# Optimization experiments

Hardware: AMD Instinct MI355X
Metric: run time of the kernel (lower is better)

Reference implementation:

```python
import jax, jax.numpy as jnp
import numpy as np

G, N, E, F, D = 4096, 64, 256, 64, 128
H1, H2 = 16, 2
EP = 32768
EPS = 1e-15
MAX_LOGSTD = 10.0


def setup_inputs() -> dict:
    key = jax.random.key(0)
    ks = jax.random.split(key, 16)
    def lin(k, i, o):
        return (jax.random.normal(k, (i, o), jnp.float32) / np.sqrt(i)).astype(jnp.float32)
    inp = {}
    inp["x"] = jax.random.normal(ks[0], (G, N, F), jnp.float32)
    inp["edge_index"] = jax.random.randint(ks[1], (G, 2, E), 0, N, dtype=jnp.int32)
    inp["edge_weight"] = jax.random.uniform(ks[2], (G, E), jnp.float32)
    inp["pos_edges"] = jax.random.randint(ks[3], (2, EP), 0, G, dtype=jnp.int32)
    inp["neg_edges"] = jax.random.randint(ks[4], (2, EP), 0, G, dtype=jnp.int32)
    inp["eps"] = jax.random.normal(ks[5], (G, D), jnp.float32)
    inp["W_gcn1"] = lin(ks[6], F, D); inp["b_gcn1"] = jnp.zeros((D,), jnp.float32)
    inp["W_fc1"] = lin(ks[7], D, H1); inp["b_fc1"] = jnp.zeros((H1,), jnp.float32)
    inp["W_fc2"] = lin(ks[8], H1, H2); inp["b_fc2"] = jnp.zeros((H2,), jnp.float32)
    inp["W_c1"] = lin(ks[9], D, 2 * D); inp["b_c1"] = jnp.zeros((2 * D,), jnp.float32)
    inp["W_mu"] = lin(ks[10], 2 * D, D); inp["b_mu"] = jnp.zeros((D,), jnp.float32)
    inp["W_ls"] = lin(ks[11], 2 * D, D); inp["b_ls"] = jnp.zeros((D,), jnp.float32)
    inp["emb"] = jax.random.normal(ks[12], (G, D), jnp.float32)
    inp["W_lin1"] = lin(ks[13], 2 * D, 2 * D); inp["b_lin1"] = jnp.zeros((2 * D,), jnp.float32)
    inp["W_lin2"] = lin(ks[14], 2 * D, 2 * D); inp["b_lin2"] = jnp.zeros((2 * D,), jnp.float32)
    return inp


def gcn_conv(x, src, dst, w, W, b, n):
    # PyG GCNConv: add self-loops (weight 1), sym-normalize, aggregate at target (col).
    xw = x @ W                                      # [n, out]
    deg = jnp.zeros((n,), xw.dtype).at[dst].add(w) + 1.0
    dinv = jax.lax.rsqrt(deg)
    norm = dinv[src] * w * dinv[dst]
    agg = jnp.zeros_like(xw).at[dst].add(xw[src] * norm[:, None])
    agg = agg + xw * (dinv * dinv)[:, None]         # self-loop term
    return agg + b


def sage_graph(x, ei, w, W_gcn1, b_gcn1, W_fc1, b_fc1, W_fc2, b_fc2):
    src, dst = ei[0], ei[1]
    h = gcn_conv(x, src, dst, w, W_gcn1, b_gcn1, N)          # [N, D]
    a1 = jnp.tanh(h @ W_fc1 + b_fc1)                         # [N, H1]
    S = jax.nn.softmax(a1 @ W_fc2 + b_fc2, axis=1)           # [N, 2]
    # get_laplacian(normalization='sym'): L = I - D^{-1/2} A D^{-1/2}, deg from row
    deg = jnp.zeros((N,), x.dtype).at[src].add(w)
    dinv = jnp.where(deg > 0, jax.lax.rsqrt(jnp.maximum(deg, 1e-30)), 0.0)
    lw = -dinv[src] * w * dinv[dst]
    L = jnp.zeros((N, N), x.dtype).at[src, dst].add(lw) + jnp.eye(N, dtype=x.dtype)
    new_adj = S.T @ (L @ S)                                  # [2, 2]
    norm_adj = new_adj / jnp.maximum(jnp.sum(jnp.abs(new_adj), axis=1, keepdims=True), 1e-12)
    diag = jnp.diagonal(norm_adj)
    pos_penalty = jnp.mean((diag - 1.0) ** 2)                # MSE vs ones(2)
    g_emb = jnp.mean(S.T @ h, axis=0)                        # [D]
    return g_emb, pos_penalty


def gcn_conv_unw(x, src, dst, W, b, n):
    return gcn_conv(x, src, dst, jnp.ones(src.shape, x.dtype), W, b, n)


def reference(x, edge_index, edge_weight, pos_edges, neg_edges, eps,
              W_gcn1, b_gcn1, W_fc1, b_fc1, W_fc2, b_fc2,
              W_c1, b_c1, W_mu, b_mu, W_ls, b_ls, emb,
              W_lin1, b_lin1, W_lin2, b_lin2):
    g_embs, pens = jax.vmap(sage_graph,
                            in_axes=(0, 0, 0, None, None, None, None, None, None))(
        x, edge_index, edge_weight, W_gcn1, b_gcn1, W_fc1, b_fc1, W_fc2, b_fc2)
    positive_penalty = jnp.mean(pens)
    # VGAE encode over graph-level graph (dropout in eval mode = identity)
    ps, pd = pos_edges[0], pos_edges[1]
    h = jax.nn.relu(gcn_conv_unw(g_embs, ps, pd, W_c1, b_c1, G))
    mu = gcn_conv_unw(h, ps, pd, W_mu, b_mu, G)
    logstd = jnp.minimum(gcn_conv_unw(h, ps, pd, W_ls, b_ls, G), MAX_LOGSTD)
    z = mu + eps * jnp.exp(logstd)                            # reparametrize
    zc = jnp.concatenate([emb, z], axis=-1)                   # [G, 2D]
    def pred(ei):
        fx = zc[ei[0]] @ W_lin1 + b_lin1
        fy = zc[ei[1]] @ W_lin2 + b_lin2
        return jax.nn.sigmoid(jnp.sum(fx * fy, axis=1))
    pos_pred = pred(pos_edges)
    neg_pred = pred(neg_edges)
    rec_loss = -jnp.mean(jnp.log(pos_pred + EPS)) - jnp.mean(jnp.log(1.0 - neg_pred + EPS))
    kl = -0.5 * jnp.mean(jnp.sum(1.0 + 2.0 * logstd - mu ** 2 - jnp.exp(2.0 * logstd), axis=1))
    pre_loss = rec_loss + kl / G
    return pre_loss, positive_penalty, pos_pred, neg_pred
```

## Files before the change

### kernel.cpp

```cpp
#include <hip/hip_runtime.h>
#include <hip/hip_bf16.h>
#include <math.h>

#define GG   4096
#define NNODE 64
#define EEDGE 256
#define FFEAT 64
#define DDIM 128
#define EP   32768

__global__ void k_prep(const float* __restrict__ Wg, const float* __restrict__ Wf1,
                       const float* __restrict__ bf1, const float* __restrict__ bg,
                       float* __restrict__ Wgf1, float* __restrict__ bcomb,
                       float* __restrict__ bg32) {
    int t = threadIdx.x;
    for (int o = t; o < 1024; o += 256) {
        int f = o >> 4, j = o & 15;
        float s = 0.f;
        for (int d = 0; d < 128; ++d) s += Wg[f * 128 + d] * Wf1[d * 16 + j];
        Wgf1[o] = s;
    }
    if (t < 16) {
        float s = bf1[t];
        for (int d = 0; d < 128; ++d) s += bg[d] * Wf1[d * 16 + t];
        bcomb[t] = s;
    }
    if (t >= 128) bg32[t - 128] = 32.0f * bg[t - 128];
}

__global__ __launch_bounds__(256) void k_xw(
    const float* __restrict__ x, const float* __restrict__ Wgf1,
    float* __restrict__ xwg)
{
    __shared__ __align__(16) float Ws[1024];
    const int t = threadIdx.x;
    for (int i = t; i < 1024; i += 256) Ws[i] = Wgf1[i];
    __syncthreads();
    const size_t r0 = (size_t)blockIdx.x * 512 + t;
    const float* x0 = x + r0 * 64;
    const float* x1 = x + (r0 + 256) * 64;
    float4 z = {0, 0, 0, 0};
    float4 c00 = z, c01 = z, c02 = z, c03 = z;
    float4 c10 = z, c11 = z, c12 = z, c13 = z;
#pragma unroll
    for (int k4 = 0; k4 < 16; ++k4) {
        float4 a0 = *(const float4*)&x0[k4 * 4];
        float4 a1 = *(const float4*)&x1[k4 * 4];
#define STEP(KK, E) { \
        const float* wr = &Ws[(k4 * 4 + (KK)) * 16]; \
        float4 w0 = *(const float4*)wr,       w1 = *(const float4*)(wr + 4); \
        float4 w2 = *(const float4*)(wr + 8), w3 = *(const float4*)(wr + 12); \
        c00.x += a0.E * w0.x; c00.y += a0.E * w0.y; c00.z += a0.E * w0.z; c00.w += a0.E * w0.w; \
        c01.x += a0.E * w1.x; c01.y += a0.E * w1.y; c01.z += a0.E * w1.z; c01.w += a0.E * w1.w; \
        c02.x += a0.E * w2.x; c02.y += a0.E * w2.y; c02.z += a0.E * w2.z; c02.w += a0.E * w2.w; \
        c03.x += a0.E * w3.x; c03.y += a0.E * w3.y; c03.z += a0.E * w3.z; c03.w += a0.E * w3.w; \
        c10.x += a1.E * w0.x; c10.y += a1.E * w0.y; c10.z += a1.E * w0.z; c10.w += a1.E * w0.w; \
        c11.x += a1.E * w1.x; c11.y += a1.E * w1.y; c11.z += a1.E * w1.z; c11.w += a1.E * w1.w; \
        c12.x += a1.E * w2.x; c12.y += a1.E * w2.y; c12.z += a1.E * w2.z; c12.w += a1.E * w2.w; \
        c13.x += a1.E * w3.x; c13.y += a1.E * w3.y; c13.z += a1.E * w3.z; c13.w += a1.E * w3.w; }
        STEP(0, x) STEP(1, y) STEP(2, z) STEP(3, w)
#undef STEP
    }
    float* o0 = &xwg[r0 * 16];
    *(float4*)&o0[0] = c00; *(float4*)&o0[4] = c01;
    *(float4*)&o0[8] = c02; *(float4*)&o0[12] = c03;
    float* o1 = &xwg[(r0 + 256) * 16];
    *(float4*)&o1[0] = c10; *(float4*)&o1[4] = c11;
    *(float4*)&o1[8] = c12; *(float4*)&o1[12] = c13;
}

__global__ __launch_bounds__(256) void k_pg(
    const float* __restrict__ x, const float* __restrict__ xwg,
    const int* __restrict__ ei, const float* __restrict__ ew,
    const float* __restrict__ bcomb,
    const float* __restrict__ Wf2, const float* __restrict__ bf2,
    float* __restrict__ Qh, float* __restrict__ pens)
{
    __shared__ __align__(16) float sm[4688];
    float* xws   = sm;
    float* a1s   = sm + 1280;
    int*   srcs  = (int*)(sm + 2304);
    int*   dsts  = (int*)(sm + 2560);
    float* lwx   = sm + 2816;
    int*   lsrc  = (int*)(sm + 3072);
    float* lnrm  = sm + 3328;
    float* enrm  = sm + 3584;
    int*   icnt  = (int*)(sm + 3840);
    int*   offs  = (int*)(sm + 3904);
    int*   curs  = (int*)(sm + 3968);
    float* degw  = sm + 4032;
    float* dinvs = sm + 4096;
    float* deg2s = sm + 4160;
    float* dinv2s= sm + 4224;
    float* wv    = sm + 4288;
    float* Ss    = sm + 4352;
    float* Ssum  = sm + 4480;
    float* LSs   = sm + 4544;
    float* bcs   = sm + 4672;

    const int g = blockIdx.x;
    const int t = threadIdx.x;

    const int* eg = ei + (size_t)g * 512;
    const int sR = eg[t];
    const int dR = eg[256 + t];
    const float wR = ew[(size_t)g * 256 + t];
    {
        int n = t >> 2, j4 = (t & 3) * 4;
        float4 v = *(const float4*)&xwg[(size_t)g * 1024 + n * 16 + j4];
        *(float4*)&xws[n * 20 + j4] = v;
    }
    srcs[t] = sR; dsts[t] = dR;
    if (t < 16) bcs[t] = bcomb[t];
    if (t < 64) { icnt[t] = 0; degw[t] = 1.0f; deg2s[t] = 0.0f; }
    if (t < 128) LSs[t] = 0.0f;
    __syncthreads();

    atomicAdd(&icnt[dR], 1);
    atomicAdd(&degw[dR], wR);
    atomicAdd(&deg2s[sR], wR);
    __syncthreads();

    if (t < 64) {
        int v = icnt[t], own = v;
        for (int o = 1; o < 64; o <<= 1) { int u = __shfl_up(v, o); if (t >= o) v += u; }
        int excl = v - own;
        offs[t] = excl; curs[t] = excl;
        dinvs[t] = rsqrtf(degw[t]);
        float dg = deg2s[t];
        dinv2s[t] = dg > 0.0f ? rsqrtf(fmaxf(dg, 1e-30f)) : 0.0f;
    }
    __syncthreads();

    {
        int pos = atomicAdd(&curs[dR], 1);
        float nm = dinvs[sR] * wR * dinvs[dR];
        lsrc[pos] = sR;
        lnrm[pos] = nm;
        enrm[t] = nm;
        lwx[t] = -dinv2s[sR] * wR * dinv2s[dR];
    }
    __syncthreads();

    {
        int n = t >> 2, j4 = (t & 3) * 4;
        float dv = dinvs[n], sc = dv * dv;
        float4 A = *(const float4*)&xws[n * 20 + j4];
        A.x *= sc; A.y *= sc; A.z *= sc; A.w *= sc;
        int o = offs[n], c = icnt[n];
        for (int j = 0; j < c; ++j) {
            int s = lsrc[o + j];
            float nm = lnrm[o + j];
            float4 X = *(const float4*)&xws[s * 20 + j4];
            A.x += X.x * nm; A.y += X.y * nm; A.z += X.z * nm; A.w += X.w * nm;
        }
        float4 bb = *(const float4*)&bcs[j4];
        a1s[n * 16 + j4 + 0] = tanhf(A.x + bb.x);
        a1s[n * 16 + j4 + 1] = tanhf(A.y + bb.y);
        a1s[n * 16 + j4 + 2] = tanhf(A.z + bb.z);
        a1s[n * 16 + j4 + 3] = tanhf(A.w + bb.w);
    }
    __syncthreads();

    if (t < 128) {
        int n = t >> 1, kk = t & 1;
        float z = bf2[kk];
#pragma unroll
        for (int j = 0; j < 16; ++j) z += a1s[n * 16 + j] * Wf2[j * 2 + kk];
        Ss[n * 2 + kk] = z;
    }
    __syncthreads();

    if (t < 64) {
        float z0 = Ss[t * 2], z1 = Ss[t * 2 + 1];
        float m = fmaxf(z0, z1);
        float e0 = expf(z0 - m), e1 = expf(z1 - m);
        float inv = 1.0f / (e0 + e1);
        e0 *= inv; e1 *= inv;
        Ss[t * 2] = e0; Ss[t * 2 + 1] = e1;
        float su = e0 + e1;
        Ssum[t] = su;
        wv[t] = dinvs[t] * dinvs[t] * su;
    }
    __syncthreads();

    for (int i = t; i < 512; i += 256) {
        int e = i >> 1, kk = i & 1;
        atomicAdd(&LSs[srcs[e] * 2 + kk], lwx[e] * Ss[dsts[e] * 2 + kk]);
    }
    atomicAdd(&wv[sR], enrm[t] * Ssum[dR]);
    __syncthreads();

    if (t < 64) {
        float s0 = Ss[t * 2], s1 = Ss[t * 2 + 1];
        float l0 = s0 + LSs[t * 2], l1 = s1 + LSs[t * 2 + 1];
        float p00 = s0 * l0, p01 = s0 * l1, p10 = s1 * l0, p11 = s1 * l1;
        for (int o = 32; o; o >>= 1) {
            p00 += __shfl_down(p00, o); p01 += __shfl_down(p01, o);
            p10 += __shfl_down(p10, o); p11 += __shfl_down(p11, o);
        }
        if (t == 0) {
            float r0 = fmaxf(fabsf(p00) + fabsf(p01), 1e-12f);
            float r1 = fmaxf(fabsf(p10) + fabsf(p11), 1e-12f);
            float d0 = p00 / r0 - 1.0f, d1 = p11 / r1 - 1.0f;
            pens[g] = 0.5f * (d0 * d0 + d1 * d1);
        }
    }
    {
        int k = t & 63, p = t >> 6;
        const float* xg = x + (size_t)g * 4096 + (p * 16) * 64 + k;
        float qk = 0.f;
#pragma unroll
        for (int n = 0; n < 16; ++n)
            qk += wv[p * 16 + n] * xg[n * 64];
        a1s[p * 64 + k] = qk;
    }
    __syncthreads();
    if (t < 64)
        Qh[(size_t)g * 64 + t] = 0.5f * (a1s[t] + a1s[64 + t] + a1s[128 + t] + a1s[192 + t]);
}

__global__ void k_cnt(const int* __restrict__ pd, int* __restrict__ icnt) {
    int e = blockIdx.x * 256 + threadIdx.x;
    atomicAdd(&icnt[pd[e]], 1);
}

__global__ void k_scan(const int* __restrict__ icnt, int* __restrict__ offs,
                       int* __restrict__ curs, float* __restrict__ dinv) {
    __shared__ int wsum[4];
    int t = threadIdx.x;
    int base = t * 16;
    int l0,l1,l2,l3,l4,l5,l6,l7,l8,l9,l10,l11,l12,l13,l14,l15;
    l0=icnt[base+0]; l1=icnt[base+1]; l2=icnt[base+2]; l3=icnt[base+3];
    l4=icnt[base+4]; l5=icnt[base+5]; l6=icnt[base+6]; l7=icnt[base+7];
    l8=icnt[base+8]; l9=icnt[base+9]; l10=icnt[base+10]; l11=icnt[base+11];
    l12=icnt[base+12]; l13=icnt[base+13]; l14=icnt[base+14]; l15=icnt[base+15];
    int s = l0+l1+l2+l3+l4+l5+l6+l7+l8+l9+l10+l11+l12+l13+l14+l15;
    int lane = t & 63, w = t >> 6;
    int v = s;
    for (int o = 1; o < 64; o <<= 1) { int u = __shfl_up(v, o); if (lane >= o) v += u; }
    if (lane == 63) wsum[w] = v;
    __syncthreads();
    int woff = 0;
    for (int i = 0; i < 4; ++i) if (i < w) woff += wsum[i];
    int run = woff + v - s;
#define SC(L, I) offs[base+(I)] = run; curs[base+(I)] = run; \
    dinv[base+(I)] = rsqrtf((float)(L) + 1.0f); run += L;
    SC(l0,0) SC(l1,1) SC(l2,2) SC(l3,3) SC(l4,4) SC(l5,5) SC(l6,6) SC(l7,7)
    SC(l8,8) SC(l9,9) SC(l10,10) SC(l11,11) SC(l12,12) SC(l13,13) SC(l14,14) SC(l15,15)
#undef SC
}

__global__ void k_place(const int* __restrict__ pe, const float* __restrict__ dinv,
                        int* __restrict__ curs, int* __restrict__ csr_src,
                        float* __restrict__ csr_nrm) {
    int e = blockIdx.x * 256 + threadIdx.x;
    int s = pe[e], d = pe[EP + e];
    int pos = atomicAdd(&curs[d], 1);
    csr_src[pos] = s;
    csr_nrm[pos] = dinv[s] * dinv[d];
}

__global__ void k_gather128(const int* __restrict__ offs, const int* __restrict__ icnt,
                            const int* __restrict__ csr_src, const float* __restrict__ csr_nrm,
                            const float* __restrict__ dinv, const float* __restrict__ in,
                            float* __restrict__ out) {
    int g = blockIdx.x, d = threadIdx.x;
    float dv = dinv[g];
    float acc = in[(size_t)g * 128 + d] * dv * dv;
    int o = offs[g], c = icnt[g];
    for (int j = 0; j < c; ++j)
        acc += in[(size_t)csr_src[o + j] * 128 + d] * csr_nrm[o + j];
    out[(size_t)g * 128 + d] = acc;
}

__global__ void k_gather256(const int* __restrict__ offs, const int* __restrict__ icnt,
                            const int* __restrict__ csr_src, const float* __restrict__ csr_nrm,
                            const float* __restrict__ dinv, const float* __restrict__ in,
                            float* __restrict__ out) {
    int g = blockIdx.x, d = threadIdx.x;
    float dv = dinv[g];
    float acc = in[(size_t)g * 256 + d] * dv * dv;
    int o = offs[g], c = icnt[g];
    for (int j = 0; j < c; ++j)
        acc += in[(size_t)csr_src[o + j] * 256 + d] * csr_nrm[o + j];
    out[(size_t)g * 256 + d] = acc;
}

__global__ __launch_bounds__(256) void k_gemm(
    const float* __restrict__ A,
    const float* __restrict__ B0, const float* __restrict__ bias0, float* __restrict__ C0,
    const float* __restrict__ B1, const float* __restrict__ bias1, float* __restrict__ C1,
    int M, int K, int N, int dorelu)
{
    __shared__ __align__(16) float lds[2 * 4352];
    const float* B = B0; const float* bias = bias0; float* C = C0;
    int by = blockIdx.y;
    if (B1 != nullptr && by >= (int)(gridDim.y >> 1)) {
        B = B1; bias = bias1; C = C1; by -= (gridDim.y >> 1);
    }
    const int mb = blockIdx.x * 64, nbb = by * 64;
    const int t = threadIdx.x;
    const int tm4 = (t >> 4) * 4, tn4 = (t & 15) * 4;
    const int ma = t >> 2, ka = (t & 3) * 8;
    const int kb = t >> 3, nb8 = (t & 7) * 8;

    float4 pa0, pa1, pb0, pb1;
#define LOADT(K0) { \
    const float* Ap = &A[(size_t)(mb + ma) * K + (K0) + ka]; \
    pa0 = *(const float4*)Ap; pa1 = *(const float4*)(Ap + 4); \
    const float* Bp = &B[(size_t)((K0) + kb) * N + nbb + nb8]; \
    pb0 = *(const float4*)Bp; pb1 = *(const float4*)(Bp + 4); }
#define STORET(BUF) { \
    float* At_ = lds + (BUF) * 4352; \
    At_[(ka + 0) * 68 + ma] = pa0.x; At_[(ka + 1) * 68 + ma] = pa0.y; \
    At_[(ka + 2) * 68 + ma] = pa0.z; At_[(ka + 3) * 68 + ma] = pa0.w; \
    At_[(ka + 4) * 68 + ma] = pa1.x; At_[(ka + 5) * 68 + ma] = pa1.y; \
    At_[(ka + 6) * 68 + ma] = pa1.z; At_[(ka + 7) * 68 + ma] = pa1.w; \
    float* Bs_ = lds + (BUF) * 4352 + 2176; \
    *(float4*)&Bs_[kb * 68 + nb8] = pb0; *(float4*)&Bs_[kb * 68 + nb8 + 4] = pb1; }

    float4 ca0 = {0,0,0,0}, ca1 = {0,0,0,0}, ca2 = {0,0,0,0}, ca3 = {0,0,0,0};
    const int nk0 = K >> 5;
    LOADT(0)
    STORET(0)
    __syncthreads();
    for (int it = 0; it < nk0; ++it) {
        if (it + 1 < nk0) LOADT((it + 1) * 32)
        const float* At_ = lds + (it & 1) * 4352;
        const float* Bs_ = At_ + 2176;
#pragma unroll
        for (int k = 0; k < 32; ++k) {
            float4 av = *(const float4*)&At_[k * 68 + tm4];
            float4 bv = *(const float4*)&Bs_[k * 68 + tn4];
            ca0.x += av.x * bv.x; ca0.y += av.x * bv.y; ca0.z += av.x * bv.z; ca0.w += av.x * bv.w;
            ca1.x += av.y * bv.x; ca1.y += av.y * bv.y; ca1.z += av.y * bv.z; ca1.w += av.y * bv.w;
            ca2.x += av.z * bv.x; ca2.y += av.z * bv.y; ca2.z += av.z * bv.z; ca2.w += av.z * bv.w;
            ca3.x += av.w * bv.x; ca3.y += av.w * bv.y; ca3.z += av.w * bv.z; ca3.w += av.w * bv.w;
        }
        if (it + 1 < nk0) {
            STORET((it + 1) & 1)
            __syncthreads();
        }
    }
#undef LOADT
#undef STORET
    float4 bv4 = {0, 0, 0, 0};
    if (bias) bv4 = *(const float4*)&bias[nbb + tn4];
#define CST(I, CV) { \
    float4 v; v.x = CV.x + bv4.x; v.y = CV.y + bv4.y; v.z = CV.z + bv4.z; v.w = CV.w + bv4.w; \
    if (dorelu) { v.x = fmaxf(v.x, 0.f); v.y = fmaxf(v.y, 0.f); v.z = fmaxf(v.z, 0.f); v.w = fmaxf(v.w, 0.f); } \
    *(float4*)&C[(size_t)(mb + tm4 + (I)) * N + nbb + tn4] = v; }
    CST(0, ca0) CST(1, ca1) CST(2, ca2) CST(3, ca3)
#undef CST
}

__global__ void k_fin_z(const float* __restrict__ mu_arr, const float* __restrict__ ls_arr,
                        const float* __restrict__ eps, const float* __restrict__ emb,
                        float* __restrict__ zc, float* __restrict__ klp) {
    __shared__ float smw[2];
    int g = blockIdx.x, d = threadIdx.x;
    int idx = g * 128 + d;
    float mu = mu_arr[idx];
    float ls = fminf(ls_arr[idx], 10.0f);
    float z = mu + eps[idx] * expf(ls);
    zc[(size_t)g * 256 + d] = emb[idx];
    zc[(size_t)g * 256 + 128 + d] = z;
    float term = 1.0f + 2.0f * ls - mu * mu - expf(2.0f * ls);
    for (int o = 32; o; o >>= 1) term += __shfl_down(term, o);
    if ((d & 63) == 0) smw[d >> 6] = term;
    __syncthreads();
    if (d == 0) klp[g] = smw[0] + smw[1];
}

__global__ void k_pred(const float* __restrict__ A, const float* __restrict__ B,
                       const int* __restrict__ pos, const int* __restrict__ neg,
                       float* __restrict__ out, float* __restrict__ predp) {
    __shared__ float smw[16];
    int t = threadIdx.x, sub = t >> 4, l = t & 15;
    int eg = blockIdx.x * 16 + sub;
    int isneg = eg >= EP;
    int e = eg - (isneg ? EP : 0);
    const int* eix = isneg ? neg : pos;
    int s = eix[e], d = eix[EP + e];
    const float4* Ar = (const float4*)(A + (size_t)s * 256);
    const float4* Br = (const float4*)(B + (size_t)d * 256);
    float dot = 0.f;
#pragma unroll
    for (int q = 0; q < 4; ++q) {
        float4 av = Ar[l + 16 * q], bv = Br[l + 16 * q];
        dot += av.x * bv.x + av.y * bv.y + av.z * bv.z + av.w * bv.w;
    }
    for (int o = 8; o; o >>= 1) dot += __shfl_down(dot, o);
    if (l == 0) {
        float p = 1.0f / (1.0f + expf(-dot));
        float term;
        if (isneg) { out[2 + EP + e] = p; term = logf(1.0f - p + 1e-15f); }
        else       { out[2 + e] = p;      term = logf(p + 1e-15f); }
        smw[sub] = term;
    }
    __syncthreads();
    if (t == 0) {
        float s16 = 0.f;
#pragma unroll
        for (int i = 0; i < 16; ++i) s16 += smw[i];
        predp[blockIdx.x] = s16;
    }
}

__global__ void k_final(const float* __restrict__ pens, const float* __restrict__ klp,
                        const float* __restrict__ predp, float* __restrict__ out) {
    __shared__ float sm[16];
    int t = threadIdx.x;
    float s_pen = 0.f, s_kl = 0.f, s_pos = 0.f, s_neg = 0.f;
    for (int i = t; i < 4096; i += 256) { s_pen += pens[i]; s_kl += klp[i]; }
    for (int i = t; i < 2048; i += 256) { s_pos += predp[i]; s_neg += predp[2048 + i]; }
    for (int o = 32; o; o >>= 1) {
        s_pen += __shfl_down(s_pen, o); s_kl += __shfl_down(s_kl, o);
        s_pos += __shfl_down(s_pos, o); s_neg += __shfl_down(s_neg, o);
    }
    int w = t >> 6;
    if ((t & 63) == 0) { sm[w] = s_pen; sm[4 + w] = s_kl; sm[8 + w] = s_pos; sm[12 + w] = s_neg; }
    __syncthreads();
    if (t == 0) {
        float pen = sm[0] + sm[1] + sm[2] + sm[3];
        float kls = sm[4] + sm[5] + sm[6] + sm[7];
        float pos = sm[8] + sm[9] + sm[10] + sm[11];
        float neg = sm[12] + sm[13] + sm[14] + sm[15];
        float rec = -(pos / 32768.0f) - (neg / 32768.0f);
        out[0] = rec - 0.5f * kls / (4096.0f * 4096.0f);
        out[1] = pen * (1.0f / 4096.0f);
    }
}

extern "C" void kernel_launch(void* const* d_in, const int* in_sizes, int n_in,
                              void* d_out, int out_size, void* d_ws, size_t ws_size,
                              hipStream_t stream) {
    const float* x   = (const float*)d_in[0];
    const int*   ei  = (const int*)d_in[1];
    const float* ew  = (const float*)d_in[2];
    const int*   pos = (const int*)d_in[3];
    const int*   neg = (const int*)d_in[4];
    const float* eps = (const float*)d_in[5];
    const float* Wg  = (const float*)d_in[6];
    const float* bg  = (const float*)d_in[7];
    const float* Wf1 = (const float*)d_in[8];
    const float* bf1 = (const float*)d_in[9];
    const float* Wf2 = (const float*)d_in[10];
    const float* bf2 = (const float*)d_in[11];
    const float* Wc1 = (const float*)d_in[12];
    const float* bc1 = (const float*)d_in[13];
    const float* Wmu = (const float*)d_in[14];
    const float* bmu = (const float*)d_in[15];
    const float* Wls = (const float*)d_in[16];
    const float* bls = (const float*)d_in[17];
    const float* emb = (const float*)d_in[18];
    const float* Wl1 = (const float*)d_in[19];
    const float* bl1 = (const float*)d_in[20];
    const float* Wl2 = (const float*)d_in[21];
    const float* bl2 = (const float*)d_in[22];
    float* out = (float*)d_out;
    float* ws  = (float*)d_ws;

    float* g_embs  = ws + 0;
    float* dinv    = ws + 524288;
    int*   icnt_g  = (int*)(ws + 528384);
    int*   off_g   = (int*)(ws + 532480);
    int*   cur_g   = (int*)(ws + 536576);
    int*   csr_src = (int*)(ws + 540672);
    float* csr_nrm = ws + 573440;
    float* Qh      = ws + 606208;
    float* ga      = ws + 868352;
    float* h       = ws + 1392640;
    float* xwg     = ws + 1392640;
    float* ha      = ws + 2441216;
    float* mu_arr  = ws + 3489792;
    float* ls_arr  = ws + 4014080;
    float* zc      = ws + 4538368;
    float* Abuf    = ws + 5586944;
    float* Bbuf    = ws + 6635520;
    float* pens    = ws + 7684096;
    float* klp     = ws + 7688192;
    float* predp   = ws + 7692288;
    float* Wgf1    = ws + 7708672;
    float* bcomb   = ws + 7709696;
    float* bg32    = ws + 7709712;

    hipMemsetAsync(icnt_g, 0, 4096u * 4, stream);

    k_prep<<<1, 256, 0, stream>>>(Wg, Wf1, bf1, bg, Wgf1, bcomb, bg32);
    k_xw<<<512, 256, 0, stream>>>(x, Wgf1, xwg);
    k_pg<<<GG, 256, 0, stream>>>(x, xwg, ei, ew, bcomb, Wf2, bf2, Qh, pens);
    k_gemm<<<dim3(64, 2), 256, 0, stream>>>(Qh, Wg, bg32, g_embs,
                                            nullptr, nullptr, nullptr, GG, 64, 128, 0);

    k_cnt<<<EP / 256, 256, 0, stream>>>(pos + EP, icnt_g);
    k_scan<<<1, 256, 0, stream>>>(icnt_g, off_g, cur_g, dinv);
    k_place<<<EP / 256, 256, 0, stream>>>(pos, dinv, cur_g, csr_src, csr_nrm);

    k_gather128<<<GG, 128, 0, stream>>>(off_g, icnt_g, csr_src, csr_nrm, dinv, g_embs, ga);
    k_gemm<<<dim3(64, 4), 256, 0, stream>>>(ga, Wc1, bc1, h,
                                            nullptr, nullptr, nullptr, GG, 128, 256, 1);

    k_gather256<<<GG, 256, 0, stream>>>(off_g, icnt_g, csr_src, csr_nrm, dinv, h, ha);
    k_gemm<<<dim3(64, 4), 256, 0, stream>>>(ha, Wmu, bmu, mu_arr,
                                            Wls, bls, ls_arr, GG, 256, 128, 0);
    k_fin_z<<<GG, 128, 0, stream>>>(mu_arr, ls_arr, eps, emb, zc, klp);

    k_gemm<<<dim3(64, 8), 256, 0, stream>>>(zc, Wl1, bl1, Abuf,
                                            Wl2, bl2, Bbuf, GG, 256, 256, 0);

    k_pred<<<(2 * EP) / 16, 256, 0, stream>>>(Abuf, Bbuf, pos, neg, out, predp);
    k_final<<<1, 256, 0, stream>>>(pens, klp, predp, out);
}
```

Measured before the change: 332.6 us.

## Fuse x@Wgf1 into per-graph kernel, stage x in LDS, shrink GEMM M-tile

Removes the separate k_xw kernel and computes each graph's x@Wgf1 inside k_pg. The graph's x tile and Wgf1 are staged in shared memory, so the global xwg write and read round trip goes away. The staged x tile is reused for the Qh reduction, which is now float4-vectorized over 16 partial rows. The generic GEMM's M-tile drops from 64 to 32 rows, doubling the grid for more blocks per launch. The cost is more LDS per k_pg block (about 36KB), which may lower occupancy, an extra barrier inside the aggregation step, and less register reuse per thread in the GEMM.

```diff
diff --git a/kernel.cpp b/kernel.cpp
--- a/kernel.cpp
+++ b/kernel.cpp
@@ -28,75 +28,35 @@
     if (t >= 128) bg32[t - 128] = 32.0f * bg[t - 128];
 }
 
-__global__ __launch_bounds__(256) void k_xw(
-    const float* __restrict__ x, const float* __restrict__ Wgf1,
-    float* __restrict__ xwg)
-{
-    __shared__ __align__(16) float Ws[1024];
-    const int t = threadIdx.x;
-    for (int i = t; i < 1024; i += 256) Ws[i] = Wgf1[i];
-    __syncthreads();
-    const size_t r0 = (size_t)blockIdx.x * 512 + t;
-    const float* x0 = x + r0 * 64;
-    const float* x1 = x + (r0 + 256) * 64;
-    float4 z = {0, 0, 0, 0};
-    float4 c00 = z, c01 = z, c02 = z, c03 = z;
-    float4 c10 = z, c11 = z, c12 = z, c13 = z;
-#pragma unroll
-    for (int k4 = 0; k4 < 16; ++k4) {
-        float4 a0 = *(const float4*)&x0[k4 * 4];
-        float4 a1 = *(const float4*)&x1[k4 * 4];
-#define STEP(KK, E) { \
-        const float* wr = &Ws[(k4 * 4 + (KK)) * 16]; \
-        float4 w0 = *(const float4*)wr,       w1 = *(const float4*)(wr + 4); \
-        float4 w2 = *(const float4*)(wr + 8), w3 = *(const float4*)(wr + 12); \
-        c00.x += a0.E * w0.x; c00.y += a0.E * w0.y; c00.z += a0.E * w0.z; c00.w += a0.E * w0.w; \
-        c01.x += a0.E * w1.x; c01.y += a0.E * w1.y; c01.z += a0.E * w1.z; c01.w += a0.E * w1.w; \
-        c02.x += a0.E * w2.x; c02.y += a0.E * w2.y; c02.z += a0.E * w2.z; c02.w += a0.E * w2.w; \
-        c03.x += a0.E * w3.x; c03.y += a0.E * w3.y; c03.z += a0.E * w3.z; c03.w += a0.E * w3.w; \
-        c10.x += a1.E * w0.x; c10.y += a1.E * w0.y; c10.z += a1.E * w0.z; c10.w += a1.E * w0.w; \
-        c11.x += a1.E * w1.x; c11.y += a1.E * w1.y; c11.z += a1.E * w1.z; c11.w += a1.E * w1.w; \
-        c12.x += a1.E * w2.x; c12.y += a1.E * w2.y; c12.z += a1.E * w2.z; c12.w += a1.E * w2.w; \
-        c13.x += a1.E * w3.x; c13.y += a1.E * w3.y; c13.z += a1.E * w3.z; c13.w += a1.E * w3.w; }
-        STEP(0, x) STEP(1, y) STEP(2, z) STEP(3, w)
-#undef STEP
-    }
-    float* o0 = &xwg[r0 * 16];
-    *(float4*)&o0[0] = c00; *(float4*)&o0[4] = c01;
-    *(float4*)&o0[8] = c02; *(float4*)&o0[12] = c03;
-    float* o1 = &xwg[(r0 + 256) * 16];
-    *(float4*)&o1[0] = c10; *(float4*)&o1[4] = c11;
-    *(float4*)&o1[8] = c12; *(float4*)&o1[12] = c13;
-}
-
 __global__ __launch_bounds__(256) void k_pg(
-    const float* __restrict__ x, const float* __restrict__ xwg,
-    const int* __restrict__ ei, const float* __restrict__ ew,
-    const float* __restrict__ bcomb,
+    const float* __restrict__ x, const int* __restrict__ ei, const float* __restrict__ ew,
+    const float* __restrict__ Wgf1, const float* __restrict__ bcomb,
     const float* __restrict__ Wf2, const float* __restrict__ bf2,
     float* __restrict__ Qh, float* __restrict__ pens)
 {
-    __shared__ __align__(16) float sm[4688];
-    float* xws   = sm;
-    float* a1s   = sm + 1280;
-    int*   srcs  = (int*)(sm + 2304);
-    int*   dsts  = (int*)(sm + 2560);
-    float* lwx   = sm + 2816;
-    int*   lsrc  = (int*)(sm + 3072);
-    float* lnrm  = sm + 3328;
-    float* enrm  = sm + 3584;
-    int*   icnt  = (int*)(sm + 3840);
-    int*   offs  = (int*)(sm + 3904);
-    int*   curs  = (int*)(sm + 3968);
-    float* degw  = sm + 4032;
-    float* dinvs = sm + 4096;
-    float* deg2s = sm + 4160;
-    float* dinv2s= sm + 4224;
-    float* wv    = sm + 4288;
-    float* Ss    = sm + 4352;
-    float* Ssum  = sm + 4480;
-    float* LSs   = sm + 4544;
-    float* bcs   = sm + 4672;
+    __shared__ __align__(16) float sm[9040];
+    float* xs    = sm;
+    float* Wgf1s = sm + 4352;
+    float* a1s   = sm + 4352;
+    float* xws   = sm + 5376;
+    int*   srcs  = (int*)(sm + 6656);
+    int*   dsts  = (int*)(sm + 6912);
+    float* lwx   = sm + 7168;
+    int*   lsrc  = (int*)(sm + 7424);
+    float* lnrm  = sm + 7680;
+    float* enrm  = sm + 7936;
+    int*   icnt  = (int*)(sm + 8192);
+    int*   offs  = (int*)(sm + 8256);
+    int*   curs  = (int*)(sm + 8320);
+    float* degw  = sm + 8384;
+    float* dinvs = sm + 8448;
+    float* deg2s = sm + 8512;
+    float* dinv2s= sm + 8576;
+    float* wv    = sm + 8640;
+    float* Ss    = sm + 8704;
+    float* Ssum  = sm + 8832;
+    float* LSs   = sm + 8896;
+    float* bcs   = sm + 9024;
 
     const int g = blockIdx.x;
     const int t = threadIdx.x;
@@ -106,9 +66,12 @@
     const int dR = eg[256 + t];
     const float wR = ew[(size_t)g * 256 + t];
     {
-        int n = t >> 2, j4 = (t & 3) * 4;
-        float4 v = *(const float4*)&xwg[(size_t)g * 1024 + n * 16 + j4];
-        *(float4*)&xws[n * 20 + j4] = v;
+        const float* xg = x + (size_t)g * 4096;
+        for (int i = t; i < 1024; i += 256) {
+            int n = i >> 4, k = (i & 15) * 4;
+            *(float4*)&xs[n * 68 + k] = *(const float4*)&xg[n * 64 + k];
+        }
+        for (int i = t; i < 1024; i += 256) Wgf1s[i] = Wgf1[i];
     }
     srcs[t] = sR; dsts[t] = dR;
     if (t < 16) bcs[t] = bcomb[t];
@@ -119,6 +82,21 @@
     atomicAdd(&icnt[dR], 1);
     atomicAdd(&degw[dR], wR);
     atomicAdd(&deg2s[sR], wR);
+    {
+        int n = t >> 2, j4 = (t & 3) * 4;
+        float4 acc = {0.f, 0.f, 0.f, 0.f};
+#pragma unroll 4
+        for (int k4 = 0; k4 < 16; ++k4) {
+            float4 xq = *(const float4*)&xs[n * 68 + k4 * 4];
+#define XWSTEP(E, KK) { \
+            float4 w = *(const float4*)&Wgf1s[(k4 * 4 + (KK)) * 16 + j4]; \
+            acc.x += xq.E * w.x; acc.y += xq.E * w.y; \
+            acc.z += xq.E * w.z; acc.w += xq.E * w.w; }
+            XWSTEP(x, 0) XWSTEP(y, 1) XWSTEP(z, 2) XWSTEP(w, 3)
+#undef XWSTEP
+        }
+        *(float4*)&xws[n * 20 + j4] = acc;
+    }
     __syncthreads();
 
     if (t < 64) {
@@ -155,6 +133,7 @@
             A.x += X.x * nm; A.y += X.y * nm; A.z += X.z * nm; A.w += X.w * nm;
         }
         float4 bb = *(const float4*)&bcs[j4];
+        __syncthreads();
         a1s[n * 16 + j4 + 0] = tanhf(A.x + bb.x);
         a1s[n * 16 + j4 + 1] = tanhf(A.y + bb.y);
         a1s[n * 16 + j4 + 2] = tanhf(A.z + bb.z);
@@ -207,17 +186,24 @@
         }
     }
     {
-        int k = t & 63, p = t >> 6;
-        const float* xg = x + (size_t)g * 4096 + (p * 16) * 64 + k;
-        float qk = 0.f;
-#pragma unroll
-        for (int n = 0; n < 16; ++n)
-            qk += wv[p * 16 + n] * xg[n * 64];
-        a1s[p * 64 + k] = qk;
-    }
-    __syncthreads();
-    if (t < 64)
-        Qh[(size_t)g * 64 + t] = 0.5f * (a1s[t] + a1s[64 + t] + a1s[128 + t] + a1s[192 + t]);
+        int p = t >> 4, k4 = (t & 15) * 4;
+        float4 q = {0.f, 0.f, 0.f, 0.f};
+#pragma unroll
+        for (int e = 0; e < 4; ++e) {
+            int n = p * 4 + e;
+            float wn = wv[n];
+            float4 xv = *(const float4*)&xs[n * 68 + k4];
+            q.x += wn * xv.x; q.y += wn * xv.y; q.z += wn * xv.z; q.w += wn * xv.w;
+        }
+        *(float4*)&a1s[p * 64 + k4] = q;
+    }
+    __syncthreads();
+    if (t < 64) {
+        float s = 0.f;
+#pragma unroll
+        for (int p = 0; p < 16; ++p) s += a1s[p * 64 + t];
+        Qh[(size_t)g * 64 + t] = 0.5f * s;
+    }
 }
 
 __global__ void k_cnt(const int* __restrict__ pd, int* __restrict__ icnt) {
@@ -293,50 +279,45 @@
     const float* __restrict__ B1, const float* __restrict__ bias1, float* __restrict__ C1,
     int M, int K, int N, int dorelu)
 {
-    __shared__ __align__(16) float lds[2 * 4352];
+    __shared__ __align__(16) float lds[2 * 3328];
     const float* B = B0; const float* bias = bias0; float* C = C0;
     int by = blockIdx.y;
     if (B1 != nullptr && by >= (int)(gridDim.y >> 1)) {
         B = B1; bias = bias1; C = C1; by -= (gridDim.y >> 1);
     }
-    const int mb = blockIdx.x * 64, nbb = by * 64;
+    const int mb = blockIdx.x * 32, nbb = by * 64;
     const int t = threadIdx.x;
-    const int tm4 = (t >> 4) * 4, tn4 = (t & 15) * 4;
-    const int ma = t >> 2, ka = (t & 3) * 8;
+    const int tm2 = (t >> 4) * 2, tn4 = (t & 15) * 4;
+    const int ma = t >> 3, ka = (t & 7) * 4;
     const int kb = t >> 3, nb8 = (t & 7) * 8;
 
-    float4 pa0, pa1, pb0, pb1;
+    float4 pa0, pb0, pb1;
 #define LOADT(K0) { \
-    const float* Ap = &A[(size_t)(mb + ma) * K + (K0) + ka]; \
-    pa0 = *(const float4*)Ap; pa1 = *(const float4*)(Ap + 4); \
+    pa0 = *(const float4*)&A[(size_t)(mb + ma) * K + (K0) + ka]; \
     const float* Bp = &B[(size_t)((K0) + kb) * N + nbb + nb8]; \
     pb0 = *(const float4*)Bp; pb1 = *(const float4*)(Bp + 4); }
 #define STORET(BUF) { \
-    float* At_ = lds + (BUF) * 4352; \
-    At_[(ka + 0) * 68 + ma] = pa0.x; At_[(ka + 1) * 68 + ma] = pa0.y; \
-    At_[(ka + 2) * 68 + ma] = pa0.z; At_[(ka + 3) * 68 + ma] = pa0.w; \
-    At_[(ka + 4) * 68 + ma] = pa1.x; At_[(ka + 5) * 68 + ma] = pa1.y; \
-    At_[(ka + 6) * 68 + ma] = pa1.z; At_[(ka + 7) * 68 + ma] = pa1.w; \
-    float* Bs_ = lds + (BUF) * 4352 + 2176; \
+    float* At_ = lds + (BUF) * 3328; \
+    At_[(ka + 0) * 36 + ma] = pa0.x; At_[(ka + 1) * 36 + ma] = pa0.y; \
+    At_[(ka + 2) * 36 + ma] = pa0.z; At_[(ka + 3) * 36 + ma] = pa0.w; \
+    float* Bs_ = lds + (BUF) * 3328 + 1152; \
     *(float4*)&Bs_[kb * 68 + nb8] = pb0; *(float4*)&Bs_[kb * 68 + nb8 + 4] = pb1; }
 
-    float4 ca0 = {0,0,0,0}, ca1 = {0,0,0,0}, ca2 = {0,0,0,0}, ca3 = {0,0,0,0};
+    float4 ca0 = {0,0,0,0}, ca1 = {0,0,0,0};
     const int nk0 = K >> 5;
     LOADT(0)
     STORET(0)
     __syncthreads();
     for (int it = 0; it < nk0; ++it) {
         if (it + 1 < nk0) LOADT((it + 1) * 32)
-        const float* At_ = lds + (it & 1) * 4352;
-        const float* Bs_ = At_ + 2176;
+        const float* At_ = lds + (it & 1) * 3328;
+        const float* Bs_ = At_ + 1152;
 #pragma unroll
         for (int k = 0; k < 32; ++k) {
-            float4 av = *(const float4*)&At_[k * 68 + tm4];
+            float2 av = *(const float2*)&At_[k * 36 + tm2];
             float4 bv = *(const float4*)&Bs_[k * 68 + tn4];
             ca0.x += av.x * bv.x; ca0.y += av.x * bv.y; ca0.z += av.x * bv.z; ca0.w += av.x * bv.w;
             ca1.x += av.y * bv.x; ca1.y += av.y * bv.y; ca1.z += av.y * bv.z; ca1.w += av.y * bv.w;
-            ca2.x += av.z * bv.x; ca2.y += av.z * bv.y; ca2.z += av.z * bv.z; ca2.w += av.z * bv.w;
-            ca3.x += av.w * bv.x; ca3.y += av.w * bv.y; ca3.z += av.w * bv.z; ca3.w += av.w * bv.w;
         }
         if (it + 1 < nk0) {
             STORET((it + 1) & 1)
@@ -350,8 +331,8 @@
 #define CST(I, CV) { \
     float4 v; v.x = CV.x + bv4.x; v.y = CV.y + bv4.y; v.z = CV.z + bv4.z; v.w = CV.w + bv4.w; \
     if (dorelu) { v.x = fmaxf(v.x, 0.f); v.y = fmaxf(v.y, 0.f); v.z = fmaxf(v.z, 0.f); v.w = fmaxf(v.w, 0.f); } \
-    *(float4*)&C[(size_t)(mb + tm4 + (I)) * N + nbb + tn4] = v; }
-    CST(0, ca0) CST(1, ca1) CST(2, ca2) CST(3, ca3)
+    *(float4*)&C[(size_t)(mb + tm2 + (I)) * N + nbb + tn4] = v; }
+    CST(0, ca0) CST(1, ca1)
 #undef CST
 }
 
@@ -472,7 +453,6 @@
     float* Qh      = ws + 606208;
     float* ga      = ws + 868352;
     float* h       = ws + 1392640;
-    float* xwg     = ws + 1392640;
     float* ha      = ws + 2441216;
     float* mu_arr  = ws + 3489792;
     float* ls_arr  = ws + 4014080;
@@ -489,26 +469,25 @@
     hipMemsetAsync(icnt_g, 0, 4096u * 4, stream);
 
     k_prep<<<1, 256, 0, stream>>>(Wg, Wf1, bf1, bg, Wgf1, bcomb, bg32);
-    k_xw<<<512, 256, 0, stream>>>(x, Wgf1, xwg);
-    k_pg<<<GG, 256, 0, stream>>>(x, xwg, ei, ew, bcomb, Wf2, bf2, Qh, pens);
-    k_gemm<<<dim3(64, 2), 256, 0, stream>>>(Qh, Wg, bg32, g_embs,
-                                            nullptr, nullptr, nullptr, GG, 64, 128, 0);
+    k_pg<<<GG, 256, 0, stream>>>(x, ei, ew, Wgf1, bcomb, Wf2, bf2, Qh, pens);
+    k_gemm<<<dim3(128, 2), 256, 0, stream>>>(Qh, Wg, bg32, g_embs,
+                                             nullptr, nullptr, nullptr, GG, 64, 128, 0);
 
     k_cnt<<<EP / 256, 256, 0, stream>>>(pos + EP, icnt_g);
     k_scan<<<1, 256, 0, stream>>>(icnt_g, off_g, cur_g, dinv);
     k_place<<<EP / 256, 256, 0, stream>>>(pos, dinv, cur_g, csr_src, csr_nrm);
 
     k_gather128<<<GG, 128, 0, stream>>>(off_g, icnt_g, csr_src, csr_nrm, dinv, g_embs, ga);
-    k_gemm<<<dim3(64, 4), 256, 0, stream>>>(ga, Wc1, bc1, h,
-                                            nullptr, nullptr, nullptr, GG, 128, 256, 1);
+    k_gemm<<<dim3(128, 4), 256, 0, stream>>>(ga, Wc1, bc1, h,
+                                             nullptr, nullptr, nullptr, GG, 128, 256, 1);
 
     k_gather256<<<GG, 256, 0, stream>>>(off_g, icnt_g, csr_src, csr_nrm, dinv, h, ha);
-    k_gemm<<<dim3(64, 4), 256, 0, stream>>>(ha, Wmu, bmu, mu_arr,
-                                            Wls, bls, ls_arr, GG, 256, 128, 0);
+    k_gemm<<<dim3(128, 4), 256, 0, stream>>>(ha, Wmu, bmu, mu_arr,
+                                             Wls, bls, ls_arr, GG, 256, 128, 0);
     k_fin_z<<<GG, 128, 0, stream>>>(mu_arr, ls_arr, eps, emb, zc, klp);
 
-    k_gemm<<<dim3(64, 8), 256, 0, stream>>>(zc, Wl1, bl1, Abuf,
-                                            Wl2, bl2, Bbuf, GG, 256, 256, 0);
+    k_gemm<<<dim3(128, 8), 256, 0, stream>>>(zc, Wl1, bl1, Abuf,
+                                             Wl2, bl2, Bbuf, GG, 256, 256, 0);
 
     k_pred<<<(2 * EP) / 16, 256, 0, stream>>>(Abuf, Bbuf, pos, neg, out, predp);
     k_final<<<1, 256, 0, stream>>>(pens, klp, predp, out);
```

Result: faster. 321.2 us (-3.4%).
